# Kernel optimization log

Hardware: AMD Instinct MI355X
Metric: run time of the kernel (lower is better)

The kernel has to match this reference:

```python
import jax, jax.numpy as jnp
import numpy as np

N_NODES = 100000
N_EDGES = 1600000
N_GRAPHS = 4096
IN_FEATS = 64
HIDDEN = 128


def setup_inputs() -> dict:
    key = jax.random.key(0)
    ks = jax.random.split(key, 16)
    feats_node = jax.random.normal(ks[0], (N_NODES, IN_FEATS), dtype=jnp.float32)
    feats_graph = jax.random.normal(ks[1], (N_GRAPHS, 3), dtype=jnp.float32)
    src = jax.random.randint(ks[2], (N_EDGES,), 0, N_NODES, dtype=jnp.int32)
    dst = jax.random.randint(ks[3], (N_EDGES,), 0, N_NODES, dtype=jnp.int32)
    node2graph = jnp.sort(jax.random.randint(ks[4], (N_NODES,), 0, N_GRAPHS, dtype=jnp.int32))
    # weights stored as [in, out] (torch Linear W.T); init per module: std=0.5 weights, bias ~ N(0.01, 0.001)
    def w(k, shape):
        return jax.random.normal(k, shape, dtype=jnp.float32) * 0.5
    def b(k, shape):
        return 0.01 + 0.001 * jax.random.normal(k, shape, dtype=jnp.float32)
    return {
        'feats_node': feats_node, 'feats_graph': feats_graph,
        'src': src, 'dst': dst, 'node2graph': node2graph,
        'W1': w(ks[5], (IN_FEATS, HIDDEN)), 'b1': b(ks[6], (HIDDEN,)),
        'W2': w(ks[7], (HIDDEN, HIDDEN)), 'b2': b(ks[8], (HIDDEN,)),
        'W3': w(ks[9], (HIDDEN, HIDDEN)), 'b3': b(ks[10], (HIDDEN,)),
        'L1w': w(ks[11], (HIDDEN + 3, 2 * HIDDEN)), 'L1b': b(ks[12], (2 * HIDDEN,)),
        'L2w': w(ks[13], (2 * HIDDEN, HIDDEN)), 'L2b': b(ks[14], (HIDDEN,)),
        'L3w': w(ks[15], (HIDDEN, 1)), 'L3b': b(jax.random.fold_in(key, 99), (1,)),
    }


def _graph_conv(x, W, b, src, dst, norm_out, norm_in):
    # DGL GraphConv(norm='both'): h_i = (sum_{j->i} x_j * d_out(j)^-1/2) * d_in(i)^-1/2 @ W + b
    m = (x * norm_out)[src]                       # [E, F] gather
    agg = jax.ops.segment_sum(m, dst, num_segments=N_NODES)
    return (agg * norm_in) @ W + b


def reference(feats_node, feats_graph, W1, b1, W2, b2, W3, b3, L1w, L1b, L2w, L2b, L3w, L3b, src, dst, node2graph):
    ones = jnp.ones((N_EDGES,), dtype=jnp.float32)
    deg_out = jax.ops.segment_sum(ones, src, num_segments=N_NODES)
    deg_in = jax.ops.segment_sum(ones, dst, num_segments=N_NODES)
    norm_out = jnp.clip(deg_out, 1.0, None)[:, None] ** -0.5  # [N,1]
    norm_in = jnp.clip(deg_in, 1.0, None)[:, None] ** -0.5

    x = jax.nn.selu(_graph_conv(feats_node, W1, b1, src, dst, norm_out, norm_in))
    x = jax.nn.selu(_graph_conv(x, W2, b2, src, dst, norm_out, norm_in))
    y_node = _graph_conv(x, W3, b3, src, dst, norm_out, norm_in)

    y_sum = jax.ops.segment_sum(y_node, node2graph, num_segments=N_GRAPHS)  # readout 'sum'
    y = jnp.concatenate([y_sum, feats_graph], axis=1)  # [G, H+3]
    y = jax.nn.selu(y @ L1w + L1b)
    y = jax.nn.selu(y @ L2w + L2b)
    return (y @ L3w + L3b).reshape(-1)
```

## Files before the change

kernel.cpp:

```cpp
#include <hip/hip_runtime.h>
#include <math.h>

#define SELU_ALPHA 1.6732632423543772f
#define SELU_SCALE 1.0507009873554805f

#define NBLK 512
#define MAXBKT 512

typedef __attribute__((ext_vector_type(8))) short bf16x8;
typedef __attribute__((ext_vector_type(4))) float f32x4;

__device__ __forceinline__ float selu_f(float x) {
    return SELU_SCALE * (x > 0.f ? x : SELU_ALPHA * expm1f(x));
}

__device__ __forceinline__ float bf2f(unsigned short u) {
    return __uint_as_float(((unsigned)u) << 16);
}
__device__ __forceinline__ unsigned short f2bf(float f) {
    unsigned u = __float_as_uint(f);
    unsigned r = (u + 0x7fffu + ((u >> 16) & 1u)) >> 16;
    return (unsigned short)r;
}

#define SCAN_B 1024

__global__ __launch_bounds__(256) void scan_block_sums(const int* __restrict__ in,
                                                       int* __restrict__ bsums, int n) {
    __shared__ int s[256];
    int b = blockIdx.x, t = threadIdx.x;
    int base = b * SCAN_B;
    int sum = 0;
    for (int i = t; i < SCAN_B; i += 256) {
        int idx = base + i;
        sum += (idx < n) ? in[idx] : 0;
    }
    s[t] = sum; __syncthreads();
    for (int off = 128; off > 0; off >>= 1) {
        if (t < off) s[t] += s[t + off];
        __syncthreads();
    }
    if (t == 0) bsums[b] = s[0];
}

__global__ __launch_bounds__(256) void scan_apply2(const int* __restrict__ in,
                                                   const int* __restrict__ bsums,
                                                   int* __restrict__ out, int n, int nb) {
    __shared__ int sb[512];
    __shared__ int s[256];
    __shared__ int blockoff;
    int b = blockIdx.x, t = threadIdx.x;

    int orig0 = (t < nb) ? bsums[t] : 0;
    int orig1 = (t + 256 < nb) ? bsums[t + 256] : 0;
    sb[t] = orig0; sb[t + 256] = orig1;
    __syncthreads();
    for (int off = 1; off < 512; off <<= 1) {
        int v0 = (t >= off) ? sb[t - off] : 0;
        int v1 = (t + 256 >= off) ? sb[t + 256 - off] : 0;
        __syncthreads();
        sb[t] += v0; sb[t + 256] += v1;
        __syncthreads();
    }
    if (t == (b & 255)) {
        bool hi = b >= 256;
        int incl = hi ? sb[t + 256] : sb[t];
        int orig = hi ? orig1 : orig0;
        blockoff = incl - orig;
    }
    __syncthreads();

    int idx0 = b * SCAN_B + t * 4;
    int v[4]; int tsum = 0;
    #pragma unroll
    for (int k = 0; k < 4; ++k) {
        int idx = idx0 + k;
        v[k] = (idx < n) ? in[idx] : 0;
        tsum += v[k];
    }
    s[t] = tsum; __syncthreads();
    for (int off = 1; off < 256; off <<= 1) {
        int x = (t >= off) ? s[t - off] : 0;
        __syncthreads();
        s[t] += x;
        __syncthreads();
    }
    int run = s[t] - tsum + blockoff;
    #pragma unroll
    for (int k = 0; k < 4; ++k) {
        int idx = idx0 + k;
        if (idx < n) out[idx] = run;
        run += v[k];
    }
}

__global__ __launch_bounds__(256) void coarse_hist_kernel(
        const int* __restrict__ src, const int* __restrict__ dst,
        int* __restrict__ cntD, int* __restrict__ cntS, int E, int nbkt) {
    __shared__ int hD[MAXBKT];
    __shared__ int hS[MAXBKT];
    int bb = blockIdx.x, t = threadIdx.x;
    for (int k = t; k < MAXBKT; k += 256) { hD[k] = 0; hS[k] = 0; }
    __syncthreads();
    int chunk = E / NBLK;
    int beg = bb * chunk, end = beg + chunk;
    for (int i = beg + t; i < end; i += 256) {
        atomicAdd(&hD[((unsigned)dst[i]) >> 8], 1);
        atomicAdd(&hS[((unsigned)src[i]) >> 8], 1);
    }
    __syncthreads();
    for (int k = t; k < nbkt; k += 256) {
        cntD[k * NBLK + bb] = hD[k];
        cntS[k * NBLK + bb] = hS[k];
    }
}

__global__ __launch_bounds__(256) void scatter_kernel(
        const int* __restrict__ src, const int* __restrict__ dst,
        const int* __restrict__ cntD, const int* __restrict__ cntS,
        uint2* __restrict__ pairs, int* __restrict__ sbufm, int E, int nbkt) {
    __shared__ int cD[MAXBKT];
    __shared__ int cS[MAXBKT];
    int bb = blockIdx.x, t = threadIdx.x;
    for (int k = t; k < nbkt; k += 256) {
        cD[k] = cntD[k * NBLK + bb];
        cS[k] = cntS[k * NBLK + bb];
    }
    __syncthreads();
    int chunk = E / NBLK;
    int beg = bb * chunk, end = beg + chunk;
    for (int i = beg + t; i < end; i += 256) {
        unsigned s = (unsigned)src[i], d = (unsigned)dst[i];
        int pD = atomicAdd(&cD[d >> 8], 1);
        pairs[pD] = make_uint2(s, d);
        int pS = atomicAdd(&cS[s >> 8], 1);
        sbufm[pS] = (int)s;
    }
}

__global__ __launch_bounds__(256) void bucket_build_kernel(
        const int* __restrict__ sbufm, const uint2* __restrict__ pairs,
        const int* __restrict__ cntD, const int* __restrict__ cntS,
        int* __restrict__ deg_out, int* __restrict__ row_start,
        int* __restrict__ deg_in, int* __restrict__ csr_src,
        int N, int E, int nbkt) {
    __shared__ int hist[256];
    __shared__ int sc[256];
    __shared__ int cur[256];
    int b = blockIdx.x, t = threadIdx.x;
    int node = (b << 8) + t;

    {
        int base = cntS[b * NBLK];
        int end = (b + 1 < nbkt) ? cntS[(b + 1) * NBLK] : 2 * E;
        hist[t] = 0; __syncthreads();
        for (int i = base + t; i < end; i += 256)
            atomicAdd(&hist[sbufm[i] & 255], 1);
        __syncthreads();
        if (node < N) deg_out[node] = hist[t];
        __syncthreads();
    }

    {
        int base = cntD[b * NBLK];
        int end = (b + 1 < nbkt) ? cntD[(b + 1) * NBLK] : E;
        hist[t] = 0; __syncthreads();
        for (int i = base + t; i < end; i += 256)
            atomicAdd(&hist[pairs[i].y & 255], 1);
        __syncthreads();
        int v = hist[t];
        sc[t] = v; __syncthreads();
        for (int off = 1; off < 256; off <<= 1) {
            int x = (t >= off) ? sc[t - off] : 0;
            __syncthreads();
            sc[t] += x;
            __syncthreads();
        }
        int ex = sc[t] - v;
        cur[t] = base + ex;
        if (node < N) { row_start[node] = base + ex; deg_in[node] = v; }
        __syncthreads();
        for (int i = base + t; i < end; i += 256) {
            uint2 p = pairs[i];
            int pos = atomicAdd(&cur[p.y & 255], 1);
            csr_src[pos] = (int)p.x;
        }
    }
}

__global__ void prep_weights_kernel(
        const float* __restrict__ W1, const float* __restrict__ W2,
        const float* __restrict__ W3, const float* __restrict__ L1w,
        const float* __restrict__ L2w,
        unsigned short* __restrict__ Wt1, unsigned short* __restrict__ Wt2,
        unsigned short* __restrict__ Wt3, unsigned short* __restrict__ L1w16,
        unsigned short* __restrict__ L2w16) {
    const int s0 = 128 * 64, s1 = 128 * 128, s2 = 128 * 128;
    const int s3 = 131 * 256 / 4, s4 = 256 * 128 / 4;
    int i = blockIdx.x * 256 + threadIdx.x;
    if (i < s0) {
        int col = i / 64, k = i % 64;
        Wt1[i] = f2bf(W1[k * 128 + col]);
        return;
    }
    i -= s0;
    if (i < s1) {
        int col = i / 128, k = i % 128;
        Wt2[i] = f2bf(W2[k * 128 + col]);
        return;
    }
    i -= s1;
    if (i < s2) {
        int col = i / 128, k = i % 128;
        Wt3[i] = f2bf(W3[k * 128 + col]);
        return;
    }
    i -= s2;
    if (i < s3) {
        float4 v = reinterpret_cast<const float4*>(L1w)[i];
        unsigned short o[4] = { f2bf(v.x), f2bf(v.y), f2bf(v.z), f2bf(v.w) };
        reinterpret_cast<uint2*>(L1w16)[i] = *reinterpret_cast<uint2*>(o);
        return;
    }
    i -= s3;
    if (i < s4) {
        float4 v = reinterpret_cast<const float4*>(L2w)[i];
        unsigned short o[4] = { f2bf(v.x), f2bf(v.y), f2bf(v.z), f2bf(v.w) };
        reinterpret_cast<uint2*>(L2w16)[i] = *reinterpret_cast<uint2*>(o);
    }
}

__global__ void cvt_feats_kernel(const float* __restrict__ feats,
                                 const int* __restrict__ deg_out,
                                 float* __restrict__ norm_out,
                                 unsigned short* __restrict__ outp, int N) {
    int i = blockIdx.x * blockDim.x + threadIdx.x;
    if (i >= 8 * N) return;
    int n = i >> 3, c = i & 7;
    float no = 1.f / sqrtf(fmaxf((float)deg_out[n], 1.f));
    if (c == 0) norm_out[n] = no;
    const float* fp = feats + (size_t)n * 64 + c * 8;
    float4 a = *reinterpret_cast<const float4*>(fp);
    float4 b = *reinterpret_cast<const float4*>(fp + 4);
    unsigned short o[8] = { f2bf(a.x * no), f2bf(a.y * no), f2bf(a.z * no), f2bf(a.w * no),
                            f2bf(b.x * no), f2bf(b.y * no), f2bf(b.z * no), f2bf(b.w * no) };
    *reinterpret_cast<float4*>(outp + (size_t)n * 64 + c * 8) = *reinterpret_cast<float4*>(o);
}

template<int TPG, int FIN>
__global__ __launch_bounds__(256) void csr_agg_kernel(
        const unsigned short* __restrict__ x, const int* __restrict__ row_start,
        const int* __restrict__ deg_in, const int* __restrict__ csr_src,
        unsigned short* __restrict__ agg, int N) {
    const int GPB = 256 / TPG;
    int g = threadIdx.x / TPG;
    int j = threadIdx.x % TPG;
    int n = blockIdx.x * GPB + g;
    if (n >= N) return;
    const int lane = threadIdx.x & 63;
    const int gbase = lane & ~(TPG - 1);
    int beg = row_start[n];
    int dg = deg_in[n];
    int end = beg + dg;
    float nin = 1.f / sqrtf(fmaxf((float)dg, 1.f));
    float acc[8] = {0.f, 0.f, 0.f, 0.f, 0.f, 0.f, 0.f, 0.f};
    int myIdx = (beg + j < end) ? csr_src[beg + j] : 0;
    for (int c = beg; c < end; c += TPG) {
        int cnt = end - c;
        int nxtIdx = (c + TPG + j < end) ? csr_src[c + TPG + j] : 0;
        float4 v[TPG];
        #pragma unroll
        for (int t = 0; t < TPG; ++t) {
            if (t < cnt) {
                int s = __shfl(myIdx, gbase + t, 64);
                v[t] = *reinterpret_cast<const float4*>(&x[(size_t)s * FIN + j * 8]);
            }
        }
        #pragma unroll
        for (int t = 0; t < TPG; ++t) {
            if (t < cnt) {
                const unsigned short* u = reinterpret_cast<const unsigned short*>(&v[t]);
                #pragma unroll
                for (int k = 0; k < 8; ++k) acc[k] += bf2f(u[k]);
            }
        }
        myIdx = nxtIdx;
    }
    unsigned short ov[8];
    #pragma unroll
    for (int k = 0; k < 8; ++k) ov[k] = f2bf(acc[k] * nin);
    *reinterpret_cast<float4*>(&agg[(size_t)n * FIN + j * 8]) = *reinterpret_cast<float4*>(ov);
}

template<int FIN, bool SELU, bool SCALE_OUT>
__global__ __launch_bounds__(256, 4) void gemm_mfma_kernel(
        const unsigned short* __restrict__ agg16,
        const unsigned short* __restrict__ Wt,
        const float* __restrict__ b,
        const float* __restrict__ norm_out,
        unsigned short* __restrict__ out,
        int N) {
    const int PAD = 8;
    const int LDW = FIN + PAD;
    const int CH = FIN / 8;
    __shared__ unsigned short sW[128 * LDW];
    const int tid = threadIdx.x;
    const int wave = tid >> 6, lane = tid & 63;
    const int wr = (wave >> 1) * 64;
    const int wc = (wave & 1) * 64;
    const int n0 = blockIdx.x * 128;

    for (int i = tid; i < 128 * CH; i += 256) {
        int col = i / CH, kc = i % CH;
        *reinterpret_cast<float4*>(&sW[col * LDW + kc * 8]) =
            *reinterpret_cast<const float4*>(&Wt[col * FIN + kc * 8]);
    }
    __syncthreads();

    const int l16 = lane & 15;
    const int lk = (lane >> 4) * 8;
    const bf16x8 zero8 = (bf16x8){0,0,0,0,0,0,0,0};
    f32x4 acc[4][4];
    #pragma unroll
    for (int mi = 0; mi < 4; ++mi)
        #pragma unroll
        for (int ci = 0; ci < 4; ++ci)
            acc[mi][ci] = (f32x4){0.f, 0.f, 0.f, 0.f};

    #pragma unroll
    for (int k0 = 0; k0 < FIN; k0 += 32) {
        bf16x8 a[4], w[4];
        #pragma unroll
        for (int mi = 0; mi < 4; ++mi) {
            int n = n0 + wr + mi * 16 + l16;
            a[mi] = (n < N)
                ? *reinterpret_cast<const bf16x8*>(&agg16[(size_t)n * FIN + k0 + lk])
                : zero8;
        }
        #pragma unroll
        for (int ci = 0; ci < 4; ++ci)
            w[ci] = *reinterpret_cast<const bf16x8*>(&sW[(wc + ci * 16 + l16) * LDW + k0 + lk]);
        #pragma unroll
        for (int mi = 0; mi < 4; ++mi)
            #pragma unroll
            for (int ci = 0; ci < 4; ++ci)
                acc[mi][ci] = __builtin_amdgcn_mfma_f32_16x16x32_bf16(
                    a[mi], w[ci], acc[mi][ci], 0, 0, 0);
    }

    const int rbase = (lane >> 4) * 4;
    #pragma unroll
    for (int ci = 0; ci < 4; ++ci) {
        int col = wc + ci * 16 + l16;
        float bias = b[col];
        #pragma unroll
        for (int mi = 0; mi < 4; ++mi) {
            #pragma unroll
            for (int r = 0; r < 4; ++r) {
                int n = n0 + wr + mi * 16 + rbase + r;
                if (n < N) {
                    float v = acc[mi][ci][r] + bias;
                    if (SELU) v = selu_f(v);
                    if (SCALE_OUT) v *= norm_out[n];
                    out[(size_t)n * 128 + col] = f2bf(v);
                }
            }
        }
    }
}

__global__ __launch_bounds__(128) void readout_kernel(
        const unsigned short* __restrict__ y, const int* __restrict__ n2g,
        float* __restrict__ gsum, int N, int G) {
    int g = blockIdx.x;
    int o = threadIdx.x;
    if (g >= G) return;
    int beg, end;
    {
        int lo = 0, hi = N;
        while (lo < hi) { int m = (lo + hi) >> 1; if (n2g[m] < g) lo = m + 1; else hi = m; }
        beg = lo;
        lo = beg; hi = N;
        while (lo < hi) { int m = (lo + hi) >> 1; if (n2g[m] < g + 1) lo = m + 1; else hi = m; }
        end = lo;
    }
    float acc = 0.f;
    for (int n = beg; n < end; ++n)
        acc += bf2f(y[(size_t)n * 128 + o]);
    gsum[(size_t)g * 128 + o] = acc;
}

__global__ __launch_bounds__(256) void mlp1_kernel(
        const float* __restrict__ gsum, const float* __restrict__ fg,
        const unsigned short* __restrict__ W16,
        const float* __restrict__ b,
        float* __restrict__ y1, int G) {
    __shared__ unsigned short sW[131 * 256];
    __shared__ float sIn[16][132];
    int tid = threadIdx.x;
    for (int i = tid; i < 131 * 256 / 2; i += 256)
        reinterpret_cast<unsigned*>(sW)[i] = reinterpret_cast<const unsigned*>(W16)[i];
    int g0 = blockIdx.x * 16;
    for (int i = tid; i < 16 * 131; i += 256) {
        int g = i / 131, k = i - g * 131;
        float v = 0.f;
        if (g0 + g < G)
            v = (k < 128) ? gsum[(size_t)(g0 + g) * 128 + k]
                          : fg[(size_t)(g0 + g) * 3 + (k - 128)];
        sIn[g][k] = v;
    }
    __syncthreads();
    float bias = b[tid];
    for (int g = 0; g < 16; ++g) {
        if (g0 + g >= G) break;
        float acc = bias;
        #pragma unroll 8
        for (int k = 0; k < 131; ++k)
            acc += sIn[g][k] * bf2f(sW[k * 256 + tid]);
        y1[(size_t)(g0 + g) * 256 + tid] = selu_f(acc);
    }
}

__global__ __launch_bounds__(256) void mlp23_kernel(
        const float* __restrict__ y1,
        const unsigned short* __restrict__ W16,
        const float* __restrict__ b2v,
        const float* __restrict__ L3w,
        const float* __restrict__ L3b,
        float* __restrict__ out, int G) {
    __shared__ unsigned short sW[256 * 128];
    __shared__ float sIn[16][256];
    __shared__ float sL3[128];
    __shared__ float red[16][2];
    int tid = threadIdx.x;
    for (int i = tid; i < 256 * 128 / 2; i += 256)
        reinterpret_cast<unsigned*>(sW)[i] = reinterpret_cast<const unsigned*>(W16)[i];
    if (tid < 128) sL3[tid] = L3w[tid];
    int g0 = blockIdx.x * 16;
    for (int i = tid; i < 16 * 256; i += 256) {
        int g = i >> 8, k = i & 255;
        sIn[g][k] = (g0 + g < G) ? y1[(size_t)(g0 + g) * 256 + k] : 0.f;
    }
    __syncthreads();
    int o = tid & 127;
    int half = tid >> 7;
    int lane = tid & 63;
    int wv = tid >> 6;
    float bias = b2v[o];
    float w3 = sL3[o];
    for (int gg = 0; gg < 8; ++gg) {
        int g = half * 8 + gg;
        float acc = bias;
        #pragma unroll 8
        for (int k = 0; k < 256; ++k)
            acc += sIn[g][k] * bf2f(sW[k * 128 + o]);
        float v = selu_f(acc) * w3;
        #pragma unroll
        for (int off = 32; off > 0; off >>= 1)
            v += __shfl_down(v, off, 64);
        if (lane == 0) red[g][wv & 1] = v;
    }
    __syncthreads();
    if (tid < 16) {
        int g = g0 + tid;
        if (g < G) out[g] = red[tid][0] + red[tid][1] + L3b[0];
    }
}

extern "C" void kernel_launch(void* const* d_in, const int* in_sizes, int n_in,
                              void* d_out, int out_size, void* d_ws, size_t ws_size,
                              hipStream_t stream) {
    const float* feats_node  = (const float*)d_in[0];
    const float* feats_graph = (const float*)d_in[1];
    const int*   src         = (const int*)d_in[2];
    const int*   dst         = (const int*)d_in[3];
    const int*   node2graph  = (const int*)d_in[4];
    const float* W1 = (const float*)d_in[5];
    const float* b1 = (const float*)d_in[6];
    const float* W2 = (const float*)d_in[7];
    const float* b2 = (const float*)d_in[8];
    const float* W3 = (const float*)d_in[9];
    const float* b3 = (const float*)d_in[10];
    const float* L1w = (const float*)d_in[11];
    const float* L1b = (const float*)d_in[12];
    const float* L2w = (const float*)d_in[13];
    const float* L2b = (const float*)d_in[14];
    const float* L3w = (const float*)d_in[15];
    const float* L3b = (const float*)d_in[16];

    const int N = in_sizes[0] / 64;
    const int G = in_sizes[1] / 3;
    const int E = in_sizes[2];
    const int NBKT = (N + 255) >> 8;
    const int nmat = NBKT * NBLK;
    const int nscan = 2 * nmat;
    const int NBsc = (nscan + SCAN_B - 1) / SCAN_B;

    int* iws = (int*)d_ws;
    int* deg_out_i = iws;
    int* deg_in_i  = deg_out_i + N;
    int* row_start = deg_in_i + N;
    int* bsums     = row_start + N;
    int* cntD      = bsums + 512;
    int* cntS      = cntD + nmat;
    int* csr_src   = cntS + nmat;

    float* norm_out = (float*)(csr_src + E);

    unsigned short* feats16 = (unsigned short*)(norm_out + N);
    unsigned short* x16     = feats16 + (size_t)N * 64;
    unsigned short* agg16   = x16 + (size_t)N * 128;
    unsigned short* y16     = agg16 + (size_t)N * 128;
    unsigned short* Wt1     = y16 + (size_t)N * 128;
    unsigned short* Wt2     = Wt1 + 128 * 64;
    unsigned short* Wt3     = Wt2 + 128 * 128;
    unsigned short* L1w16   = Wt3 + 128 * 128;
    unsigned short* L2w16   = L1w16 + 131 * 256;

    float* gsum = (float*)(L2w16 + 256 * 128);
    float* y1   = gsum + (size_t)G * 128;

    uint2* pairs = (uint2*)(((uintptr_t)y16 + 15) & ~(uintptr_t)15);
    int*   sbuf  = (int*)(pairs + E);
    int*   sbufm = sbuf - E;

    float* out = (float*)d_out;

    {
        const int total = 128 * 64 + 2 * 128 * 128 + 131 * 256 / 4 + 256 * 128 / 4;
        prep_weights_kernel<<<(total + 255) / 256, 256, 0, stream>>>(
            W1, W2, W3, L1w, L2w, Wt1, Wt2, Wt3, L1w16, L2w16);
    }

    coarse_hist_kernel<<<NBLK, 256, 0, stream>>>(src, dst, cntD, cntS, E, NBKT);
    scan_block_sums<<<NBsc, 256, 0, stream>>>(cntD, bsums, nscan);
    scan_apply2<<<NBsc, 256, 0, stream>>>(cntD, bsums, cntD, nscan, NBsc);
    scatter_kernel<<<NBLK, 256, 0, stream>>>(src, dst, cntD, cntS, pairs, sbufm, E, NBKT);

    bucket_build_kernel<<<NBKT, 256, 0, stream>>>(
        sbufm, pairs, cntD, cntS, deg_out_i, row_start, deg_in_i, csr_src, N, E, NBKT);

    cvt_feats_kernel<<<(8 * N + 255) / 256, 256, 0, stream>>>(
        feats_node, deg_out_i, norm_out, feats16, N);

    const int gemm_grid = (N + 127) / 128;

    csr_agg_kernel<8, 64><<<(N + 31) / 32, 256, 0, stream>>>(
        feats16, row_start, deg_in_i, csr_src, agg16, N);
    gemm_mfma_kernel<64, true, true><<<gemm_grid, 256, 0, stream>>>(
        agg16, Wt1, b1, norm_out, x16, N);

    csr_agg_kernel<16, 128><<<(N + 15) / 16, 256, 0, stream>>>(
        x16, row_start, deg_in_i, csr_src, agg16, N);
    gemm_mfma_kernel<128, true, true><<<gemm_grid, 256, 0, stream>>>(
        agg16, Wt2, b2, norm_out, x16, N);

    csr_agg_kernel<16, 128><<<(N + 15) / 16, 256, 0, stream>>>(
        x16, row_start, deg_in_i, csr_src, agg16, N);
    gemm_mfma_kernel<128, false, false><<<gemm_grid, 256, 0, stream>>>(
        agg16, Wt3, b3, norm_out, y16, N);

    readout_kernel<<<G, 128, 0, stream>>>(y16, node2graph, gsum, N, G);

    mlp1_kernel<<<(G + 15) / 16, 256, 0, stream>>>(gsum, feats_graph, L1w16, L1b, y1, G);
    mlp23_kernel<<<(G + 15) / 16, 256, 0, stream>>>(
        y1, L2w16, L2b, L3w, L3b, out, G);
}
```

Measured before the change: 423.4 us.

## Fuse weight prep into histogram, feature cast into bucket build, pack edge pairs

Weight conversion now runs as extra blocks of the histogram kernel, and the feature scaling and bf16 cast moves into the bucket-build kernel, which already holds per-node out-degree in shared memory. Together these remove two kernel launches and the deg_out round trip through memory. Edge pairs shrink from 8 to 4 bytes by packing the low 8 bits of dst with a 24-bit src, halving scatter and bucket traffic. The packing assumes node ids fit in 24 bits, and the feature cast now runs on only NBKT (~391) blocks, which could limit parallelism for that part.

```diff
diff --git a/kernel.cpp b/kernel.cpp
--- a/kernel.cpp
+++ b/kernel.cpp
@@ -94,9 +94,39 @@
     }
 }
 
-__global__ __launch_bounds__(256) void coarse_hist_kernel(
+__global__ __launch_bounds__(256) void hist_prep_kernel(
         const int* __restrict__ src, const int* __restrict__ dst,
-        int* __restrict__ cntD, int* __restrict__ cntS, int E, int nbkt) {
+        int* __restrict__ cntD, int* __restrict__ cntS, int E, int nbkt,
+        const float* __restrict__ W1, const float* __restrict__ W2,
+        const float* __restrict__ W3, const float* __restrict__ L1w,
+        const float* __restrict__ L2w,
+        unsigned short* __restrict__ Wt1, unsigned short* __restrict__ Wt2,
+        unsigned short* __restrict__ Wt3, unsigned short* __restrict__ L1w16,
+        unsigned short* __restrict__ L2w16) {
+    if (blockIdx.x >= NBLK) {
+        const int s0 = 128 * 64, s1 = 128 * 128, s2 = 128 * 128;
+        const int s3 = 131 * 256 / 4, s4 = 256 * 128 / 4;
+        int i = (blockIdx.x - NBLK) * 256 + threadIdx.x;
+        if (i < s0) { int col = i / 64, k = i % 64; Wt1[i] = f2bf(W1[k * 128 + col]); return; }
+        i -= s0;
+        if (i < s1) { int col = i / 128, k = i % 128; Wt2[i] = f2bf(W2[k * 128 + col]); return; }
+        i -= s1;
+        if (i < s2) { int col = i / 128, k = i % 128; Wt3[i] = f2bf(W3[k * 128 + col]); return; }
+        i -= s2;
+        if (i < s3) {
+            float4 v = reinterpret_cast<const float4*>(L1w)[i];
+            unsigned short o[4] = { f2bf(v.x), f2bf(v.y), f2bf(v.z), f2bf(v.w) };
+            reinterpret_cast<uint2*>(L1w16)[i] = *reinterpret_cast<uint2*>(o);
+            return;
+        }
+        i -= s3;
+        if (i < s4) {
+            float4 v = reinterpret_cast<const float4*>(L2w)[i];
+            unsigned short o[4] = { f2bf(v.x), f2bf(v.y), f2bf(v.z), f2bf(v.w) };
+            reinterpret_cast<uint2*>(L2w16)[i] = *reinterpret_cast<uint2*>(o);
+        }
+        return;
+    }
     __shared__ int hD[MAXBKT];
     __shared__ int hS[MAXBKT];
     int bb = blockIdx.x, t = threadIdx.x;
@@ -118,7 +148,7 @@
 __global__ __launch_bounds__(256) void scatter_kernel(
         const int* __restrict__ src, const int* __restrict__ dst,
         const int* __restrict__ cntD, const int* __restrict__ cntS,
-        uint2* __restrict__ pairs, int* __restrict__ sbufm, int E, int nbkt) {
+        unsigned* __restrict__ pairs, int* __restrict__ sbufm, int E, int nbkt) {
     __shared__ int cD[MAXBKT];
     __shared__ int cS[MAXBKT];
     int bb = blockIdx.x, t = threadIdx.x;
@@ -132,23 +162,26 @@
     for (int i = beg + t; i < end; i += 256) {
         unsigned s = (unsigned)src[i], d = (unsigned)dst[i];
         int pD = atomicAdd(&cD[d >> 8], 1);
-        pairs[pD] = make_uint2(s, d);
+        pairs[pD] = s | ((d & 255u) << 24);
         int pS = atomicAdd(&cS[s >> 8], 1);
         sbufm[pS] = (int)s;
     }
 }
 
 __global__ __launch_bounds__(256) void bucket_build_kernel(
-        const int* __restrict__ sbufm, const uint2* __restrict__ pairs,
+        const int* __restrict__ sbufm, const unsigned* __restrict__ pairs,
         const int* __restrict__ cntD, const int* __restrict__ cntS,
-        int* __restrict__ deg_out, int* __restrict__ row_start,
-        int* __restrict__ deg_in, int* __restrict__ csr_src,
-        int N, int E, int nbkt) {
+        const float* __restrict__ feats,
+        float* __restrict__ norm_out, unsigned short* __restrict__ feats16,
+        int* __restrict__ row_start, int* __restrict__ deg_in,
+        int* __restrict__ csr_src, int N, int E, int nbkt) {
     __shared__ int hist[256];
     __shared__ int sc[256];
     __shared__ int cur[256];
+    __shared__ float nrm[256];
     int b = blockIdx.x, t = threadIdx.x;
     int node = (b << 8) + t;
+    int node0 = b << 8;
 
     {
         int base = cntS[b * NBLK];
@@ -157,7 +190,25 @@
         for (int i = base + t; i < end; i += 256)
             atomicAdd(&hist[sbufm[i] & 255], 1);
         __syncthreads();
-        if (node < N) deg_out[node] = hist[t];
+        float no = 1.f / sqrtf(fmaxf((float)hist[t], 1.f));
+        nrm[t] = no;
+        if (node < N) norm_out[node] = no;
+        __syncthreads();
+    }
+
+    {
+        int cnt = min(256, N - node0);
+        for (int i = t; i < cnt * 8; i += 256) {
+            int nl = i >> 3, c = i & 7;
+            float no = nrm[nl];
+            const float* fp = feats + (size_t)(node0 + nl) * 64 + c * 8;
+            float4 a = *reinterpret_cast<const float4*>(fp);
+            float4 bv = *reinterpret_cast<const float4*>(fp + 4);
+            unsigned short o[8] = { f2bf(a.x * no), f2bf(a.y * no), f2bf(a.z * no), f2bf(a.w * no),
+                                    f2bf(bv.x * no), f2bf(bv.y * no), f2bf(bv.z * no), f2bf(bv.w * no) };
+            *reinterpret_cast<float4*>(feats16 + (size_t)(node0 + nl) * 64 + c * 8) =
+                *reinterpret_cast<float4*>(o);
+        }
         __syncthreads();
     }
 
@@ -166,7 +217,7 @@
         int end = (b + 1 < nbkt) ? cntD[(b + 1) * NBLK] : E;
         hist[t] = 0; __syncthreads();
         for (int i = base + t; i < end; i += 256)
-            atomicAdd(&hist[pairs[i].y & 255], 1);
+            atomicAdd(&hist[(pairs[i] >> 24) & 255], 1);
         __syncthreads();
         int v = hist[t];
         sc[t] = v; __syncthreads();
@@ -181,70 +232,11 @@
         if (node < N) { row_start[node] = base + ex; deg_in[node] = v; }
         __syncthreads();
         for (int i = base + t; i < end; i += 256) {
-            uint2 p = pairs[i];
-            int pos = atomicAdd(&cur[p.y & 255], 1);
-            csr_src[pos] = (int)p.x;
-        }
-    }
-}
-
-__global__ void prep_weights_kernel(
-        const float* __restrict__ W1, const float* __restrict__ W2,
-        const float* __restrict__ W3, const float* __restrict__ L1w,
-        const float* __restrict__ L2w,
-        unsigned short* __restrict__ Wt1, unsigned short* __restrict__ Wt2,
-        unsigned short* __restrict__ Wt3, unsigned short* __restrict__ L1w16,
-        unsigned short* __restrict__ L2w16) {
-    const int s0 = 128 * 64, s1 = 128 * 128, s2 = 128 * 128;
-    const int s3 = 131 * 256 / 4, s4 = 256 * 128 / 4;
-    int i = blockIdx.x * 256 + threadIdx.x;
-    if (i < s0) {
-        int col = i / 64, k = i % 64;
-        Wt1[i] = f2bf(W1[k * 128 + col]);
-        return;
-    }
-    i -= s0;
-    if (i < s1) {
-        int col = i / 128, k = i % 128;
-        Wt2[i] = f2bf(W2[k * 128 + col]);
-        return;
-    }
-    i -= s1;
-    if (i < s2) {
-        int col = i / 128, k = i % 128;
-        Wt3[i] = f2bf(W3[k * 128 + col]);
-        return;
-    }
-    i -= s2;
-    if (i < s3) {
-        float4 v = reinterpret_cast<const float4*>(L1w)[i];
-        unsigned short o[4] = { f2bf(v.x), f2bf(v.y), f2bf(v.z), f2bf(v.w) };
-        reinterpret_cast<uint2*>(L1w16)[i] = *reinterpret_cast<uint2*>(o);
-        return;
-    }
-    i -= s3;
-    if (i < s4) {
-        float4 v = reinterpret_cast<const float4*>(L2w)[i];
-        unsigned short o[4] = { f2bf(v.x), f2bf(v.y), f2bf(v.z), f2bf(v.w) };
-        reinterpret_cast<uint2*>(L2w16)[i] = *reinterpret_cast<uint2*>(o);
-    }
-}
-
-__global__ void cvt_feats_kernel(const float* __restrict__ feats,
-                                 const int* __restrict__ deg_out,
-                                 float* __restrict__ norm_out,
-                                 unsigned short* __restrict__ outp, int N) {
-    int i = blockIdx.x * blockDim.x + threadIdx.x;
-    if (i >= 8 * N) return;
-    int n = i >> 3, c = i & 7;
-    float no = 1.f / sqrtf(fmaxf((float)deg_out[n], 1.f));
-    if (c == 0) norm_out[n] = no;
-    const float* fp = feats + (size_t)n * 64 + c * 8;
-    float4 a = *reinterpret_cast<const float4*>(fp);
-    float4 b = *reinterpret_cast<const float4*>(fp + 4);
-    unsigned short o[8] = { f2bf(a.x * no), f2bf(a.y * no), f2bf(a.z * no), f2bf(a.w * no),
-                            f2bf(b.x * no), f2bf(b.y * no), f2bf(b.z * no), f2bf(b.w * no) };
-    *reinterpret_cast<float4*>(outp + (size_t)n * 64 + c * 8) = *reinterpret_cast<float4*>(o);
+            unsigned p = pairs[i];
+            int pos = atomicAdd(&cur[(p >> 24) & 255], 1);
+            csr_src[pos] = (int)(p & 0xFFFFFFu);
+        }
+    }
 }
 
 template<int TPG, int FIN>
@@ -497,8 +489,7 @@
     const int NBsc = (nscan + SCAN_B - 1) / SCAN_B;
 
     int* iws = (int*)d_ws;
-    int* deg_out_i = iws;
-    int* deg_in_i  = deg_out_i + N;
+    int* deg_in_i  = iws;
     int* row_start = deg_in_i + N;
     int* bsums     = row_start + N;
     int* cntD      = bsums + 512;
@@ -520,28 +511,27 @@
     float* gsum = (float*)(L2w16 + 256 * 128);
     float* y1   = gsum + (size_t)G * 128;
 
-    uint2* pairs = (uint2*)(((uintptr_t)y16 + 15) & ~(uintptr_t)15);
-    int*   sbuf  = (int*)(pairs + E);
-    int*   sbufm = sbuf - E;
+    unsigned* pairs = (unsigned*)(((uintptr_t)y16 + 15) & ~(uintptr_t)15);
+    int*      sbuf  = (int*)(pairs + E);
+    int*      sbufm = sbuf - E;
 
     float* out = (float*)d_out;
 
     {
-        const int total = 128 * 64 + 2 * 128 * 128 + 131 * 256 / 4 + 256 * 128 / 4;
-        prep_weights_kernel<<<(total + 255) / 256, 256, 0, stream>>>(
+        const int wtotal = 128 * 64 + 2 * 128 * 128 + 131 * 256 / 4 + 256 * 128 / 4;
+        const int wblocks = (wtotal + 255) / 256;
+        hist_prep_kernel<<<NBLK + wblocks, 256, 0, stream>>>(
+            src, dst, cntD, cntS, E, NBKT,
             W1, W2, W3, L1w, L2w, Wt1, Wt2, Wt3, L1w16, L2w16);
     }
 
-    coarse_hist_kernel<<<NBLK, 256, 0, stream>>>(src, dst, cntD, cntS, E, NBKT);
     scan_block_sums<<<NBsc, 256, 0, stream>>>(cntD, bsums, nscan);
     scan_apply2<<<NBsc, 256, 0, stream>>>(cntD, bsums, cntD, nscan, NBsc);
     scatter_kernel<<<NBLK, 256, 0, stream>>>(src, dst, cntD, cntS, pairs, sbufm, E, NBKT);
 
     bucket_build_kernel<<<NBKT, 256, 0, stream>>>(
-        sbufm, pairs, cntD, cntS, deg_out_i, row_start, deg_in_i, csr_src, N, E, NBKT);
-
-    cvt_feats_kernel<<<(8 * N + 255) / 256, 256, 0, stream>>>(
-        feats_node, deg_out_i, norm_out, feats16, N);
+        sbufm, pairs, cntD, cntS, feats_node,
+        norm_out, feats16, row_start, deg_in_i, csr_src, N, E, NBKT);
 
     const int gemm_grid = (N + 127) / 128;
 
```

New measurement: 416.9 us. About the same (-1.5%).
